# Kernel optimization log

Measured on AMD Instinct MI355X. Metric: run time of the kernel, lower is better.

Reference implementation:

```python
import jax, jax.numpy as jnp
import numpy as np

B, D, T = 32, 384, 4096   # batch, latent_dim, sequence length
K = 256                   # codebook size
BETA = 0.25               # commitment weight


def setup_inputs() -> dict:
    key = jax.random.key(0)
    k1, k2 = jax.random.split(key)
    z = jax.random.normal(k1, (B, D, T), dtype=jnp.float32)
    codebook = jax.random.normal(k2, (K, D), dtype=jnp.float32)
    return {"z": z, "codebook": codebook}


def reference(z, codebook):
    # z: [B, D, T] -> x: [B, T, D]  (the module's permute(0,2,1))
    x = jnp.transpose(z, (0, 2, 1))
    # squared euclidean distance to every code: [B, T, K]
    x2 = jnp.sum(x * x, axis=-1, keepdims=True)            # [B,T,1]
    e2 = jnp.sum(codebook * codebook, axis=-1)             # [K]
    dist = x2 - 2.0 * jnp.einsum('btd,kd->btk', x, codebook) + e2
    indices = jnp.argmin(dist, axis=-1)                    # [B,T] int
    quantize = codebook[indices]                           # gather [B,T,D]
    # commitment loss: beta * mse(stop_grad(quantize), x)
    loss = BETA * jnp.mean(jnp.square(jax.lax.stop_gradient(quantize) - x))
    # straight-through estimator
    quantize = x + jax.lax.stop_gradient(quantize - x)
    # permute back to [B, D, T]
    return jnp.transpose(quantize, (0, 2, 1)), indices, loss
```

## Files before the change

### kernel.cpp

```cpp
#include <hip/hip_runtime.h>

constexpr int BB = 32;
constexpr int DD = 384;
constexpr int TN = 4096;
constexpr int KK = 256;
constexpr float BETA = 0.25f;

constexpr int TT  = 64;
constexpr int DG  = DD / 4;
constexpr int ECH = 4;
constexpr int NCH = DG / ECH;

constexpr size_t QSIZE = (size_t)BB * DD * TN;
constexpr size_t ISIZE = (size_t)BB * TN;

__global__ void e2_kernel(const float* __restrict__ cb, float* __restrict__ e2) {
    int c = threadIdx.x;
    const float4* row = (const float4*)(cb + (size_t)c * DD);
    float s = 0.f;
    #pragma unroll
    for (int g = 0; g < DG; ++g) {
        float4 v = row[g];
        s += v.x * v.x + v.y * v.y + v.z * v.z + v.w * v.w;
    }
    e2[c] = s;
}

__global__ __launch_bounds__(256, 2)
void vq_kernel(const float* __restrict__ z, const float* __restrict__ cb,
               const float* __restrict__ e2g, float* __restrict__ out) {
    __shared__ float4 es4[ECH][KK];
    __shared__ float4 xs4[ECH][TT];
    __shared__ float  e2s[KK];
    __shared__ int    idxs[TT];
    __shared__ float  wsum[4];

    const int tid = threadIdx.x;
    const int bid = blockIdx.x;
    const int b   = bid >> 6;
    const int t0  = (bid & 63) * TT;

    const int tx = tid & 31;
    const int ty = tid >> 5;

    e2s[tid] = e2g[tid];

    const float*  zb  = z + (size_t)b * DD * TN + t0;
    const float4* cb4 = (const float4*)cb;

    const int xr  = tid >> 6;
    const int xtt = tid & 63;

    float acc[8][8];
    #pragma unroll
    for (int i = 0; i < 8; ++i)
        #pragma unroll
        for (int j = 0; j < 8; ++j) acc[i][j] = 0.f;

    for (int ch = 0; ch < NCH; ++ch) {
        const int dgb = ch * ECH;
        float4 ev0 = cb4[(size_t)tid * DG + dgb + 0];
        float4 ev1 = cb4[(size_t)tid * DG + dgb + 1];
        float4 ev2 = cb4[(size_t)tid * DG + dgb + 2];
        float4 ev3 = cb4[(size_t)tid * DG + dgb + 3];
        float x0 = zb[(size_t)(4 * (dgb + xr) + 0) * TN + xtt];
        float x1 = zb[(size_t)(4 * (dgb + xr) + 1) * TN + xtt];
        float x2 = zb[(size_t)(4 * (dgb + xr) + 2) * TN + xtt];
        float x3 = zb[(size_t)(4 * (dgb + xr) + 3) * TN + xtt];
        __syncthreads();
        es4[0][tid] = ev0;
        es4[1][tid] = ev1;
        es4[2][tid] = ev2;
        es4[3][tid] = ev3;
        xs4[xr][xtt] = make_float4(x0, x1, x2, x3);
        __syncthreads();

        #pragma unroll
        for (int dgl = 0; dgl < ECH; ++dgl) {
            float4 xv[8];
            #pragma unroll
            for (int i = 0; i < 8; ++i) xv[i] = xs4[dgl][ty * 8 + i];
            #pragma unroll
            for (int j = 0; j < 8; ++j) {
                float4 ev = es4[dgl][tx + 32 * j];
                #pragma unroll
                for (int i = 0; i < 8; ++i) {
                    acc[i][j] += xv[i].x * ev.x;
                    acc[i][j] += xv[i].y * ev.y;
                    acc[i][j] += xv[i].z * ev.z;
                    acc[i][j] += xv[i].w * ev.w;
                }
            }
        }
    }

    float bv[8]; int bi[8];
    #pragma unroll
    for (int i = 0; i < 8; ++i) { bv[i] = 3.4e38f; bi[i] = 0x7fffffff; }
    #pragma unroll
    for (int j = 0; j < 8; ++j) {
        const int c = tx + 32 * j;
        const float e2c = e2s[c];
        #pragma unroll
        for (int i = 0; i < 8; ++i) {
            float v = e2c - 2.f * acc[i][j];
            if (v < bv[i]) { bv[i] = v; bi[i] = c; }
        }
    }
    #pragma unroll
    for (int m = 16; m >= 1; m >>= 1) {
        #pragma unroll
        for (int i = 0; i < 8; ++i) {
            float ov = __shfl_xor(bv[i], m, 64);
            int   oi = __shfl_xor(bi[i], m, 64);
            if (ov < bv[i] || (ov == bv[i] && oi < bi[i])) { bv[i] = ov; bi[i] = oi; }
        }
    }
    if (tx == 0) {
        #pragma unroll
        for (int i = 0; i < 8; ++i) idxs[ty * 8 + i] = bi[i];
    }
    __syncthreads();

    {
        const int myi = idxs[xtt];
        const float4* crow = cb4 + (size_t)myi * DG;
        float* outq = out + (size_t)b * DD * TN + t0;
        float lsum = 0.f;
        #pragma unroll
        for (int m = 0; m < 24; ++m) {
            int dg = xr + 4 * m;
            float4 q = crow[dg];
            float x0 = zb[(size_t)(4 * dg + 0) * TN + xtt];
            float x1 = zb[(size_t)(4 * dg + 1) * TN + xtt];
            float x2 = zb[(size_t)(4 * dg + 2) * TN + xtt];
            float x3 = zb[(size_t)(4 * dg + 3) * TN + xtt];
            float d0 = q.x - x0, d1 = q.y - x1, d2 = q.z - x2, d3 = q.w - x3;
            lsum += d0 * d0 + d1 * d1 + d2 * d2 + d3 * d3;
            outq[(size_t)(4 * dg + 0) * TN + xtt] = q.x;
            outq[(size_t)(4 * dg + 1) * TN + xtt] = q.y;
            outq[(size_t)(4 * dg + 2) * TN + xtt] = q.z;
            outq[(size_t)(4 * dg + 3) * TN + xtt] = q.w;
        }
        if (tid < TT)
            out[QSIZE + (size_t)b * TN + t0 + tid] = (float)idxs[tid];

        #pragma unroll
        for (int m = 32; m >= 1; m >>= 1) lsum += __shfl_xor(lsum, m, 64);
        if ((tid & 63) == 0) wsum[tid >> 6] = lsum;
        __syncthreads();
        if (tid == 0) {
            float s = wsum[0] + wsum[1] + wsum[2] + wsum[3];
            atomicAdd(out + QSIZE + ISIZE,
                      s * (BETA / (float)((size_t)BB * DD * TN)));
        }
    }
}

extern "C" void kernel_launch(void* const* d_in, const int* in_sizes, int n_in,
                              void* d_out, int out_size, void* d_ws, size_t ws_size,
                              hipStream_t stream) {
    (void)in_sizes; (void)n_in; (void)out_size; (void)ws_size;
    const float* z  = (const float*)d_in[0];
    const float* cb = (const float*)d_in[1];
    float* out  = (float*)d_out;
    float* e2ws = (float*)d_ws;

    hipMemsetAsync(out + QSIZE + ISIZE, 0, sizeof(float), stream);
    e2_kernel<<<dim3(1), dim3(256), 0, stream>>>(cb, e2ws);
    vq_kernel<<<dim3(BB * (TN / TT)), dim3(256), 0, stream>>>(z, cb, e2ws, out);
}
```

Baseline: 698.8 us.

## Double-buffer codebook and z chunks with direct global-to-LDS loads

The main loop now double-buffers the codebook and z tiles in shared memory. The codebook chunk for the next step is fetched with global_load_lds straight into LDS, and the z values are prefetched into registers, both while the current chunk is being computed. This halves the barriers per chunk and hides load latency behind the FMA work. Separately, the e2 precompute is parallelised to one wavefront per code, and it zeroes the loss slot, which removes the memset launch. The cost is doubled shared memory and more register pressure, which could reduce occupancy at the 2-blocks-per-SIMD launch bound.

```diff
diff --git a/kernel.cpp b/kernel.cpp
--- a/kernel.cpp
+++ b/kernel.cpp
@@ -14,23 +14,34 @@
 constexpr size_t QSIZE = (size_t)BB * DD * TN;
 constexpr size_t ISIZE = (size_t)BB * TN;
 
-__global__ void e2_kernel(const float* __restrict__ cb, float* __restrict__ e2) {
-    int c = threadIdx.x;
+__device__ __forceinline__ void gl_lds16(const float4* g, float4* l) {
+    __builtin_amdgcn_global_load_lds(
+        (const __attribute__((address_space(1))) void*)g,
+        (__attribute__((address_space(3))) void*)l, 16, 0, 0);
+}
+
+__global__ void e2_kernel(const float* __restrict__ cb, float* __restrict__ e2,
+                          float* __restrict__ loss_slot) {
+    const int c = blockIdx.x;
+    const int l = threadIdx.x;
     const float4* row = (const float4*)(cb + (size_t)c * DD);
-    float s = 0.f;
+    float4 v = row[l];
+    float s = v.x * v.x + v.y * v.y + v.z * v.z + v.w * v.w;
+    if (l < DG - 64) {
+        float4 w = row[64 + l];
+        s += w.x * w.x + w.y * w.y + w.z * w.z + w.w * w.w;
+    }
     #pragma unroll
-    for (int g = 0; g < DG; ++g) {
-        float4 v = row[g];
-        s += v.x * v.x + v.y * v.y + v.z * v.z + v.w * v.w;
-    }
-    e2[c] = s;
+    for (int m = 32; m >= 1; m >>= 1) s += __shfl_xor(s, m, 64);
+    if (l == 0) e2[c] = s;
+    if (c == 0 && l == 0) *loss_slot = 0.f;
 }
 
 __global__ __launch_bounds__(256, 2)
 void vq_kernel(const float* __restrict__ z, const float* __restrict__ cb,
                const float* __restrict__ e2g, float* __restrict__ out) {
-    __shared__ float4 es4[ECH][KK];
-    __shared__ float4 xs4[ECH][TT];
+    __shared__ float4 es4[2][ECH][KK];
+    __shared__ float4 xs4[2][ECH][TT];
     __shared__ float  e2s[KK];
     __shared__ int    idxs[TT];
     __shared__ float  wsum[4];
@@ -42,6 +53,7 @@
 
     const int tx = tid & 31;
     const int ty = tid >> 5;
+    const int wb = tid & ~63;
 
     e2s[tid] = e2g[tid];
 
@@ -51,6 +63,18 @@
     const int xr  = tid >> 6;
     const int xtt = tid & 63;
 
+    {
+        #pragma unroll
+        for (int dgl = 0; dgl < ECH; ++dgl)
+            gl_lds16(&cb4[(size_t)tid * DG + dgl], &es4[0][dgl][wb]);
+        float x0 = zb[(size_t)(4 * xr + 0) * TN + xtt];
+        float x1 = zb[(size_t)(4 * xr + 1) * TN + xtt];
+        float x2 = zb[(size_t)(4 * xr + 2) * TN + xtt];
+        float x3 = zb[(size_t)(4 * xr + 3) * TN + xtt];
+        xs4[0][xr][xtt] = make_float4(x0, x1, x2, x3);
+    }
+    __syncthreads();
+
     float acc[8][8];
     #pragma unroll
     for (int i = 0; i < 8; ++i)
@@ -58,31 +82,28 @@
         for (int j = 0; j < 8; ++j) acc[i][j] = 0.f;
 
     for (int ch = 0; ch < NCH; ++ch) {
-        const int dgb = ch * ECH;
-        float4 ev0 = cb4[(size_t)tid * DG + dgb + 0];
-        float4 ev1 = cb4[(size_t)tid * DG + dgb + 1];
-        float4 ev2 = cb4[(size_t)tid * DG + dgb + 2];
-        float4 ev3 = cb4[(size_t)tid * DG + dgb + 3];
-        float x0 = zb[(size_t)(4 * (dgb + xr) + 0) * TN + xtt];
-        float x1 = zb[(size_t)(4 * (dgb + xr) + 1) * TN + xtt];
-        float x2 = zb[(size_t)(4 * (dgb + xr) + 2) * TN + xtt];
-        float x3 = zb[(size_t)(4 * (dgb + xr) + 3) * TN + xtt];
-        __syncthreads();
-        es4[0][tid] = ev0;
-        es4[1][tid] = ev1;
-        es4[2][tid] = ev2;
-        es4[3][tid] = ev3;
-        xs4[xr][xtt] = make_float4(x0, x1, x2, x3);
-        __syncthreads();
+        const int cur = ch & 1, nxt = cur ^ 1;
+        const bool pf = (ch + 1 < NCH);
+        float x0, x1, x2, x3;
+        if (pf) {
+            const int dgb = (ch + 1) * ECH;
+            x0 = zb[(size_t)(4 * (dgb + xr) + 0) * TN + xtt];
+            x1 = zb[(size_t)(4 * (dgb + xr) + 1) * TN + xtt];
+            x2 = zb[(size_t)(4 * (dgb + xr) + 2) * TN + xtt];
+            x3 = zb[(size_t)(4 * (dgb + xr) + 3) * TN + xtt];
+            #pragma unroll
+            for (int dgl = 0; dgl < ECH; ++dgl)
+                gl_lds16(&cb4[(size_t)tid * DG + dgb + dgl], &es4[nxt][dgl][wb]);
+        }
 
         #pragma unroll
         for (int dgl = 0; dgl < ECH; ++dgl) {
             float4 xv[8];
             #pragma unroll
-            for (int i = 0; i < 8; ++i) xv[i] = xs4[dgl][ty * 8 + i];
+            for (int i = 0; i < 8; ++i) xv[i] = xs4[cur][dgl][ty * 8 + i];
             #pragma unroll
             for (int j = 0; j < 8; ++j) {
-                float4 ev = es4[dgl][tx + 32 * j];
+                float4 ev = es4[cur][dgl][tx + 32 * j];
                 #pragma unroll
                 for (int i = 0; i < 8; ++i) {
                     acc[i][j] += xv[i].x * ev.x;
@@ -92,6 +113,9 @@
                 }
             }
         }
+
+        if (pf) xs4[nxt][xr][xtt] = make_float4(x0, x1, x2, x3);
+        __syncthreads();
     }
 
     float bv[8]; int bi[8];
@@ -166,7 +190,6 @@
     float* out  = (float*)d_out;
     float* e2ws = (float*)d_ws;
 
-    hipMemsetAsync(out + QSIZE + ISIZE, 0, sizeof(float), stream);
-    e2_kernel<<<dim3(1), dim3(256), 0, stream>>>(cb, e2ws);
+    e2_kernel<<<dim3(KK), dim3(64), 0, stream>>>(cb, e2ws, out + QSIZE + ISIZE);
     vq_kernel<<<dim3(BB * (TN / TT)), dim3(256), 0, stream>>>(z, cb, e2ws, out);
 }
```

New measurement: 1.942 ms. 178% more time.
